# Kernel optimization log

Hardware: AMD Instinct MI355X
Metric: run time of the kernel (lower is better)

The kernel has to match this reference:

```python
import jax, jax.numpy as jnp
import numpy as np

BATCH = 8
IN_FEATURES = 4096
OUT_FEATURES = 16384


def setup_inputs() -> dict:
    key = jax.random.key(0)
    k1, k2, k3 = jax.random.split(key, 3)
    # activations, fp16 (w4a16 path)
    x = jax.random.normal(k1, (BATCH, IN_FEATURES), dtype=jnp.float16)
    # packed int4 weights: each element holds two signed 4-bit values
    # (low nibble = even column 2k, high nibble = odd column 2k+1)
    weight = jax.random.randint(k2, (OUT_FEATURES, IN_FEATURES // 2), 0, 256, dtype=jnp.int32)
    # per-output-channel symmetric scales (small positive values)
    weight_scales = (jax.random.uniform(k3, (OUT_FEATURES,), dtype=jnp.float16) * jnp.float16(0.01)
                     + jnp.float16(0.001))
    return {"x": x, "weight": weight, "weight_scales": weight_scales}


def _dequant_i4(weight, scales):
    """Unpack two signed int4 per byte and apply per-row scales.
    weight: [out, in//2] int32 (byte values 0..255); scales: [out] fp16.
    Returns [out, in] in scales.dtype.
    """
    low = weight & 0xF
    high = (weight >> 4) & 0xF
    # sign-extend 4-bit two's complement (the torch module stores signed int4;
    # mask 0x88 XOR in the kernel is the equivalent sign-bit flip)
    low = jnp.where(low >= 8, low - 16, low)
    high = jnp.where(high >= 8, high - 16, high)
    w = jnp.stack([low, high], axis=-1).reshape(weight.shape[0], -1)  # [out, in]
    return w.astype(scales.dtype) * scales[:, None]


def reference(x, weight, weight_scales):
    W = _dequant_i4(weight, weight_scales)           # [out, in] fp16
    return jnp.matmul(x, W.T)                         # [batch, out] fp16
```

## Files before the change

### kernel.cpp

```cpp
#include <hip/hip_runtime.h>
#include <stdint.h>

#define BATCH 8
#define K_DIM 4096
#define N_DIM 16384
#define KH (K_DIM / 2)
#define NPAIR (K_DIM / 2)
#define BLOCK 512
#define ROWS_PER_WAVE 4
#define ROWS_PER_BLOCK 32
#define ITERS (KH / 4 / 64)

typedef _Float16 h2 __attribute__((ext_vector_type(2)));
typedef int i4 __attribute__((ext_vector_type(4)));

__device__ __forceinline__ h2 as_h2(uint32_t u) { return __builtin_bit_cast(h2, u); }

__device__ __forceinline__ float fdot2f(h2 a, h2 b, float c) {
    return __builtin_amdgcn_fdot2(a, b, c, false);
}

__global__ __launch_bounds__(BLOCK, 4)
void w4a16_gemv(const float* __restrict__ x,
                const int*   __restrict__ w,
                const float* __restrict__ scales,
                float*       __restrict__ out)
{
    __shared__ uint4 xchunks[2 * NPAIR];
    const int tid = threadIdx.x;
    const int wave = tid >> 6;
    const int lane = tid & 63;
    const int row0 = blockIdx.x * ROWS_PER_BLOCK + wave * ROWS_PER_WAVE;

    const i4* __restrict__ wv0 = (const i4*)(w + (size_t)(row0 + 0) * KH);
    const i4* __restrict__ wv1 = (const i4*)(w + (size_t)(row0 + 1) * KH);
    const i4* __restrict__ wv2 = (const i4*)(w + (size_t)(row0 + 2) * KH);
    const i4* __restrict__ wv3 = (const i4*)(w + (size_t)(row0 + 3) * KH);

    int qwA[4][4], qwB[4][4];

    auto loadset = [&](int (&qw)[4][4], int t) {
        const int u = (t << 6) + lane;
        const i4 a = __builtin_nontemporal_load(wv0 + u);
        const i4 b = __builtin_nontemporal_load(wv1 + u);
        const i4 c = __builtin_nontemporal_load(wv2 + u);
        const i4 d = __builtin_nontemporal_load(wv3 + u);
        qw[0][0] = a[0]; qw[0][1] = a[1]; qw[0][2] = a[2]; qw[0][3] = a[3];
        qw[1][0] = b[0]; qw[1][1] = b[1]; qw[1][2] = b[2]; qw[1][3] = b[3];
        qw[2][0] = c[0]; qw[2][1] = c[1]; qw[2][2] = c[2]; qw[2][3] = c[3];
        qw[3][0] = d[0]; qw[3][1] = d[1]; qw[3][2] = d[2]; qw[3][3] = d[3];
    };

    loadset(qwA, 0);
    loadset(qwB, 1);

    #pragma unroll
    for (int it = 0; it < NPAIR / 2 / BLOCK; ++it) {
        const int q = it * BLOCK + tid;
        uint32_t pk0[BATCH], pk1[BATCH];
        #pragma unroll
        for (int b = 0; b < BATCH; ++b) {
            const float4 v = *reinterpret_cast<const float4*>(x + (size_t)b * K_DIM + 4 * q);
            pk0[b] = __builtin_bit_cast(uint32_t, __builtin_amdgcn_cvt_pkrtz(v.x, v.y));
            pk1[b] = __builtin_bit_cast(uint32_t, __builtin_amdgcn_cvt_pkrtz(v.z, v.w));
        }
        const int c0 = 4 * q;
        const int s = (q >> 1) & 7;
        xchunks[(c0 + 0) ^ s] = make_uint4(pk0[0], pk0[1], pk0[2], pk0[3]);
        xchunks[(c0 + 1) ^ s] = make_uint4(pk0[4], pk0[5], pk0[6], pk0[7]);
        xchunks[(c0 + 2) ^ s] = make_uint4(pk1[0], pk1[1], pk1[2], pk1[3]);
        xchunks[(c0 + 3) ^ s] = make_uint4(pk1[4], pk1[5], pk1[6], pk1[7]);
    }
    __syncthreads();

    float acc[ROWS_PER_WAVE][BATCH];
    #pragma unroll
    for (int j = 0; j < ROWS_PER_WAVE; ++j)
        #pragma unroll
        for (int b = 0; b < BATCH; ++b) acc[j][b] = 0.0f;

    const h2 neg1032 = as_h2(0xE408E408u);

    auto compute = [&](int (&qw)[4][4], int t) {
        const int u = (t << 6) + lane;
        const int cbase = u << 3;
        const int xork = u & 7;
        #pragma unroll
        for (int m = 0; m < 4; ++m) {
            const uint4 xa = xchunks[cbase + ((2 * m)     ^ xork)];
            const uint4 xb = xchunks[cbase + ((2 * m + 1) ^ xork)];
            #pragma unroll
            for (int j = 0; j < ROWS_PER_WAVE; ++j) {
                const uint32_t bv = (uint32_t)qw[j][m];
                const uint32_t tt = (bv & 0xFu) | ((bv << 12) & 0x000F0000u);
                const h2 w2 = as_h2(tt ^ 0x64086408u) + neg1032;
                acc[j][0] = fdot2f(w2, as_h2(xa.x), acc[j][0]);
                acc[j][1] = fdot2f(w2, as_h2(xa.y), acc[j][1]);
                acc[j][2] = fdot2f(w2, as_h2(xa.z), acc[j][2]);
                acc[j][3] = fdot2f(w2, as_h2(xa.w), acc[j][3]);
                acc[j][4] = fdot2f(w2, as_h2(xb.x), acc[j][4]);
                acc[j][5] = fdot2f(w2, as_h2(xb.y), acc[j][5]);
                acc[j][6] = fdot2f(w2, as_h2(xb.z), acc[j][6]);
                acc[j][7] = fdot2f(w2, as_h2(xb.w), acc[j][7]);
            }
        }
    };

    #pragma unroll 1
    for (int t = 0; t < ITERS - 2; t += 2) {
        compute(qwA, t);
        loadset(qwA, t + 2);
        compute(qwB, t + 1);
        loadset(qwB, t + 3);
    }
    compute(qwA, ITERS - 2);
    compute(qwB, ITERS - 1);

    float vals[32];
    #pragma unroll
    for (int j = 0; j < ROWS_PER_WAVE; ++j)
        #pragma unroll
        for (int b = 0; b < BATCH; ++b) vals[j * 8 + b] = acc[j][b];

    #pragma unroll
    for (int k = 0; k < 5; ++k) {
        const int sel = (lane >> k) & 1;
        const int n = 32 >> k;
        #pragma unroll
        for (int i = 0; i < n / 2; ++i) {
            const float a = vals[2 * i];
            const float c = vals[2 * i + 1];
            const float mine  = sel ? c : a;
            const float other = sel ? a : c;
            vals[i] = mine + __shfl_xor(other, 1 << k, 64);
        }
    }
    const float total = vals[0] + __shfl_xor(vals[0], 32, 64);

    if (lane < 32) {
        const int r = row0 + (lane >> 3);
        out[(size_t)(lane & 7) * N_DIM + r] = total * scales[r];
    }
}

extern "C" void kernel_launch(void* const* d_in, const int* in_sizes, int n_in,
                              void* d_out, int out_size, void* d_ws, size_t ws_size,
                              hipStream_t stream) {
    const float* x      = (const float*)d_in[0];
    const int*   w      = (const int*)d_in[1];
    const float* scales = (const float*)d_in[2];
    float*       out    = (float*)d_out;

    dim3 grid(N_DIM / ROWS_PER_BLOCK);
    dim3 block(BLOCK);
    hipLaunchKernelGGL(w4a16_gemv, grid, block, 0, stream, x, w, scales, out);
}
```

Baseline: 197.2 us.

## Split K across two blocks with fewer rows per wave and add reduce kernel

Each row's K dimension is now split between two blocks, and each wave handles 2 rows instead of 4. This gives four times as many blocks and higher occupancy (launch bounds raised to 8). Partial sums go to a workspace buffer, and a second kernel adds the two halves and applies the per-row scales. The trade-off is an extra launch, extra global traffic for the partials, and the x staging and conversion now being repeated in twice as many blocks.

```diff
diff --git a/kernel.cpp b/kernel.cpp
--- a/kernel.cpp
+++ b/kernel.cpp
@@ -5,11 +5,12 @@
 #define K_DIM 4096
 #define N_DIM 16384
 #define KH (K_DIM / 2)
-#define NPAIR (K_DIM / 2)
+#define KHH (KH / 2)
+#define NPAIRH (K_DIM / 4)
 #define BLOCK 512
-#define ROWS_PER_WAVE 4
-#define ROWS_PER_BLOCK 32
-#define ITERS (KH / 4 / 64)
+#define ROWS_PER_WAVE 2
+#define ROWS_PER_BLOCK 16
+#define ITERS (KHH / 4 / 64)
 
 typedef _Float16 h2 __attribute__((ext_vector_type(2)));
 typedef int i4 __attribute__((ext_vector_type(4)));
@@ -20,47 +21,41 @@
     return __builtin_amdgcn_fdot2(a, b, c, false);
 }
 
-__global__ __launch_bounds__(BLOCK, 4)
-void w4a16_gemv(const float* __restrict__ x,
-                const int*   __restrict__ w,
-                const float* __restrict__ scales,
-                float*       __restrict__ out)
+__global__ __launch_bounds__(BLOCK, 8)
+void w4a16_gemv_split(const float* __restrict__ x,
+                      const int*   __restrict__ w,
+                      float*       __restrict__ partial)
 {
-    __shared__ uint4 xchunks[2 * NPAIR];
-    const int tid = threadIdx.x;
+    __shared__ uint4 xchunks[2 * NPAIRH];
+    const int tid  = threadIdx.x;
     const int wave = tid >> 6;
     const int lane = tid & 63;
-    const int row0 = blockIdx.x * ROWS_PER_BLOCK + wave * ROWS_PER_WAVE;
+    const int z    = blockIdx.x;
+    const int half = z & 1;
+    const int row0 = (z >> 1) * ROWS_PER_BLOCK + wave * ROWS_PER_WAVE;
 
-    const i4* __restrict__ wv0 = (const i4*)(w + (size_t)(row0 + 0) * KH);
-    const i4* __restrict__ wv1 = (const i4*)(w + (size_t)(row0 + 1) * KH);
-    const i4* __restrict__ wv2 = (const i4*)(w + (size_t)(row0 + 2) * KH);
-    const i4* __restrict__ wv3 = (const i4*)(w + (size_t)(row0 + 3) * KH);
+    const i4* __restrict__ wv0 = (const i4*)(w + (size_t)(row0 + 0) * KH + half * KHH);
+    const i4* __restrict__ wv1 = (const i4*)(w + (size_t)(row0 + 1) * KH + half * KHH);
 
-    int qwA[4][4], qwB[4][4];
-
-    auto loadset = [&](int (&qw)[4][4], int t) {
+    int qwc[2][4], qwn[2][4];
+    auto loadset = [&](int (&qw)[2][4], int t) {
         const int u = (t << 6) + lane;
         const i4 a = __builtin_nontemporal_load(wv0 + u);
         const i4 b = __builtin_nontemporal_load(wv1 + u);
-        const i4 c = __builtin_nontemporal_load(wv2 + u);
-        const i4 d = __builtin_nontemporal_load(wv3 + u);
         qw[0][0] = a[0]; qw[0][1] = a[1]; qw[0][2] = a[2]; qw[0][3] = a[3];
         qw[1][0] = b[0]; qw[1][1] = b[1]; qw[1][2] = b[2]; qw[1][3] = b[3];
-        qw[2][0] = c[0]; qw[2][1] = c[1]; qw[2][2] = c[2]; qw[2][3] = c[3];
-        qw[3][0] = d[0]; qw[3][1] = d[1]; qw[3][2] = d[2]; qw[3][3] = d[3];
     };
 
-    loadset(qwA, 0);
-    loadset(qwB, 1);
+    loadset(qwc, 0);
+    loadset(qwn, 1);
 
-    #pragma unroll
-    for (int it = 0; it < NPAIR / 2 / BLOCK; ++it) {
-        const int q = it * BLOCK + tid;
+    {
+        const int q = tid;
         uint32_t pk0[BATCH], pk1[BATCH];
         #pragma unroll
         for (int b = 0; b < BATCH; ++b) {
-            const float4 v = *reinterpret_cast<const float4*>(x + (size_t)b * K_DIM + 4 * q);
+            const float4 v = *reinterpret_cast<const float4*>(
+                x + (size_t)b * K_DIM + half * (K_DIM / 2) + 4 * q);
             pk0[b] = __builtin_bit_cast(uint32_t, __builtin_amdgcn_cvt_pkrtz(v.x, v.y));
             pk1[b] = __builtin_bit_cast(uint32_t, __builtin_amdgcn_cvt_pkrtz(v.z, v.w));
         }
@@ -81,7 +76,7 @@
 
     const h2 neg1032 = as_h2(0xE408E408u);
 
-    auto compute = [&](int (&qw)[4][4], int t) {
+    auto compute = [&](int (&qw)[2][4], int t) {
         const int u = (t << 6) + lane;
         const int cbase = u << 3;
         const int xork = u & 7;
@@ -106,26 +101,23 @@
         }
     };
 
-    #pragma unroll 1
-    for (int t = 0; t < ITERS - 2; t += 2) {
-        compute(qwA, t);
-        loadset(qwA, t + 2);
-        compute(qwB, t + 1);
-        loadset(qwB, t + 3);
-    }
-    compute(qwA, ITERS - 2);
-    compute(qwB, ITERS - 1);
+    compute(qwc, 0);
+    loadset(qwc, 2);
+    compute(qwn, 1);
+    loadset(qwn, 3);
+    compute(qwc, 2);
+    compute(qwn, 3);
 
-    float vals[32];
+    float vals[16];
     #pragma unroll
     for (int j = 0; j < ROWS_PER_WAVE; ++j)
         #pragma unroll
         for (int b = 0; b < BATCH; ++b) vals[j * 8 + b] = acc[j][b];
 
     #pragma unroll
-    for (int k = 0; k < 5; ++k) {
+    for (int k = 0; k < 4; ++k) {
         const int sel = (lane >> k) & 1;
-        const int n = 32 >> k;
+        const int n = 16 >> k;
         #pragma unroll
         for (int i = 0; i < n / 2; ++i) {
             const float a = vals[2 * i];
@@ -135,12 +127,31 @@
             vals[i] = mine + __shfl_xor(other, 1 << k, 64);
         }
     }
-    const float total = vals[0] + __shfl_xor(vals[0], 32, 64);
+    const float t1 = vals[0] + __shfl_xor(vals[0], 16, 64);
+    const float total = t1 + __shfl_xor(t1, 32, 64);
 
-    if (lane < 32) {
+    if (lane < 16) {
         const int r = row0 + (lane >> 3);
-        out[(size_t)(lane & 7) * N_DIM + r] = total * scales[r];
+        partial[(size_t)((half << 3) + (lane & 7)) * N_DIM + r] = total;
     }
+}
+
+__global__ __launch_bounds__(256)
+void w4a16_reduce(const float* __restrict__ partial,
+                  const float* __restrict__ scales,
+                  float*       __restrict__ out)
+{
+    const int idx4 = (blockIdx.x * 256 + threadIdx.x) * 4;
+    const int r = idx4 & (N_DIM - 1);
+    const float4 p0 = *reinterpret_cast<const float4*>(partial + idx4);
+    const float4 p1 = *reinterpret_cast<const float4*>(partial + (size_t)BATCH * N_DIM + idx4);
+    const float4 sc = *reinterpret_cast<const float4*>(scales + r);
+    float4 o;
+    o.x = (p0.x + p1.x) * sc.x;
+    o.y = (p0.y + p1.y) * sc.y;
+    o.z = (p0.z + p1.z) * sc.z;
+    o.w = (p0.w + p1.w) * sc.w;
+    *reinterpret_cast<float4*>(out + idx4) = o;
 }
 
 extern "C" void kernel_launch(void* const* d_in, const int* in_sizes, int n_in,
@@ -150,8 +161,13 @@
     const int*   w      = (const int*)d_in[1];
     const float* scales = (const float*)d_in[2];
     float*       out    = (float*)d_out;
+    float*       part   = (float*)d_ws;
 
-    dim3 grid(N_DIM / ROWS_PER_BLOCK);
-    dim3 block(BLOCK);
-    hipLaunchKernelGGL(w4a16_gemv, grid, block, 0, stream, x, w, scales, out);
+    dim3 grid1(2 * N_DIM / ROWS_PER_BLOCK);
+    dim3 block1(BLOCK);
+    hipLaunchKernelGGL(w4a16_gemv_split, grid1, block1, 0, stream, x, w, part);
+
+    dim3 grid2(BATCH * N_DIM / 4 / 256);
+    dim3 block2(256);
+    hipLaunchKernelGGL(w4a16_reduce, grid2, block2, 0, stream, part, scales, out);
 }
```

New measurement: 193.9 us. About the same (-1.7%).

## Split K across wave pairs and halve rows per block

Applied to the files above, without the earlier changes.

Each pair of waves now shares the same four output rows, with each wave handling half of the K dimension. The partial sums are combined through shared memory after a block barrier. Rows per block drop from 32 to 16, which doubles the grid size and the number of times x is staged into LDS. The weight loads also change: they now use plain loads instead of nontemporal ones, and the double buffer becomes a single prefetch buffer. The intent is more parallelism and shorter per-wave loops, at the cost of redundant x conversion work and an extra sync.

```diff
diff --git a/kernel.cpp b/kernel.cpp
--- a/kernel.cpp
+++ b/kernel.cpp
@@ -5,11 +5,11 @@
 #define K_DIM 4096
 #define N_DIM 16384
 #define KH (K_DIM / 2)
-#define NPAIR (K_DIM / 2)
+#define KHH (KH / 2)
 #define BLOCK 512
 #define ROWS_PER_WAVE 4
-#define ROWS_PER_BLOCK 32
-#define ITERS (KH / 4 / 64)
+#define ROWS_PER_BLOCK 16
+#define ITERS (KHH / 4 / 64)
 
 typedef _Float16 h2 __attribute__((ext_vector_type(2)));
 typedef int i4 __attribute__((ext_vector_type(4)));
@@ -26,36 +26,36 @@
                 const float* __restrict__ scales,
                 float*       __restrict__ out)
 {
-    __shared__ uint4 xchunks[2 * NPAIR];
-    const int tid = threadIdx.x;
+    __shared__ uint4 xchunks[K_DIM];
+    __shared__ float sred[4][32];
+    const int tid  = threadIdx.x;
     const int wave = tid >> 6;
     const int lane = tid & 63;
-    const int row0 = blockIdx.x * ROWS_PER_BLOCK + wave * ROWS_PER_WAVE;
+    const int hh   = wave & 1;
+    const int row0 = blockIdx.x * ROWS_PER_BLOCK + (wave >> 1) * ROWS_PER_WAVE;
 
-    const i4* __restrict__ wv0 = (const i4*)(w + (size_t)(row0 + 0) * KH);
-    const i4* __restrict__ wv1 = (const i4*)(w + (size_t)(row0 + 1) * KH);
-    const i4* __restrict__ wv2 = (const i4*)(w + (size_t)(row0 + 2) * KH);
-    const i4* __restrict__ wv3 = (const i4*)(w + (size_t)(row0 + 3) * KH);
+    const i4* __restrict__ wv0 = (const i4*)(w + (size_t)(row0 + 0) * KH + hh * KHH);
+    const i4* __restrict__ wv1 = (const i4*)(w + (size_t)(row0 + 1) * KH + hh * KHH);
+    const i4* __restrict__ wv2 = (const i4*)(w + (size_t)(row0 + 2) * KH + hh * KHH);
+    const i4* __restrict__ wv3 = (const i4*)(w + (size_t)(row0 + 3) * KH + hh * KHH);
 
-    int qwA[4][4], qwB[4][4];
-
-    auto loadset = [&](int (&qw)[4][4], int t) {
+    int qw[4][4];
+    auto loadset = [&](int (&q)[4][4], int t) {
         const int u = (t << 6) + lane;
-        const i4 a = __builtin_nontemporal_load(wv0 + u);
-        const i4 b = __builtin_nontemporal_load(wv1 + u);
-        const i4 c = __builtin_nontemporal_load(wv2 + u);
-        const i4 d = __builtin_nontemporal_load(wv3 + u);
-        qw[0][0] = a[0]; qw[0][1] = a[1]; qw[0][2] = a[2]; qw[0][3] = a[3];
-        qw[1][0] = b[0]; qw[1][1] = b[1]; qw[1][2] = b[2]; qw[1][3] = b[3];
-        qw[2][0] = c[0]; qw[2][1] = c[1]; qw[2][2] = c[2]; qw[2][3] = c[3];
-        qw[3][0] = d[0]; qw[3][1] = d[1]; qw[3][2] = d[2]; qw[3][3] = d[3];
+        const i4 a = wv0[u];
+        const i4 b = wv1[u];
+        const i4 c = wv2[u];
+        const i4 d = wv3[u];
+        q[0][0] = a[0]; q[0][1] = a[1]; q[0][2] = a[2]; q[0][3] = a[3];
+        q[1][0] = b[0]; q[1][1] = b[1]; q[1][2] = b[2]; q[1][3] = b[3];
+        q[2][0] = c[0]; q[2][1] = c[1]; q[2][2] = c[2]; q[2][3] = c[3];
+        q[3][0] = d[0]; q[3][1] = d[1]; q[3][2] = d[2]; q[3][3] = d[3];
     };
 
-    loadset(qwA, 0);
-    loadset(qwB, 1);
+    loadset(qw, 0);
 
     #pragma unroll
-    for (int it = 0; it < NPAIR / 2 / BLOCK; ++it) {
+    for (int it = 0; it < K_DIM / 4 / BLOCK; ++it) {
         const int q = it * BLOCK + tid;
         uint32_t pk0[BATCH], pk1[BATCH];
         #pragma unroll
@@ -81,9 +81,10 @@
 
     const h2 neg1032 = as_h2(0xE408E408u);
 
-    auto compute = [&](int (&qw)[4][4], int t) {
+    const int coff = hh << 11;
+    auto compute = [&](int (&q)[4][4], int t) {
         const int u = (t << 6) + lane;
-        const int cbase = u << 3;
+        const int cbase = coff + (u << 3);
         const int xork = u & 7;
         #pragma unroll
         for (int m = 0; m < 4; ++m) {
@@ -91,7 +92,7 @@
             const uint4 xb = xchunks[cbase + ((2 * m + 1) ^ xork)];
             #pragma unroll
             for (int j = 0; j < ROWS_PER_WAVE; ++j) {
-                const uint32_t bv = (uint32_t)qw[j][m];
+                const uint32_t bv = (uint32_t)q[j][m];
                 const uint32_t tt = (bv & 0xFu) | ((bv << 12) & 0x000F0000u);
                 const h2 w2 = as_h2(tt ^ 0x64086408u) + neg1032;
                 acc[j][0] = fdot2f(w2, as_h2(xa.x), acc[j][0]);
@@ -107,14 +108,16 @@
     };
 
     #pragma unroll 1
-    for (int t = 0; t < ITERS - 2; t += 2) {
-        compute(qwA, t);
-        loadset(qwA, t + 2);
-        compute(qwB, t + 1);
-        loadset(qwB, t + 3);
+    for (int t = 0; t < ITERS - 1; ++t) {
+        int nq[4][4];
+        loadset(nq, t + 1);
+        compute(qw, t);
+        #pragma unroll
+        for (int j = 0; j < 4; ++j)
+            #pragma unroll
+            for (int m = 0; m < 4; ++m) qw[j][m] = nq[j][m];
     }
-    compute(qwA, ITERS - 2);
-    compute(qwB, ITERS - 1);
+    compute(qw, ITERS - 1);
 
     float vals[32];
     #pragma unroll
@@ -137,9 +140,12 @@
     }
     const float total = vals[0] + __shfl_xor(vals[0], 32, 64);
 
-    if (lane < 32) {
+    if (hh && lane < 32) sred[wave >> 1][lane] = total;
+    __syncthreads();
+    if (!hh && lane < 32) {
+        const float s2 = total + sred[wave >> 1][lane];
         const int r = row0 + (lane >> 3);
-        out[(size_t)(lane & 7) * N_DIM + r] = total * scales[r];
+        out[(size_t)(lane & 7) * N_DIM + r] = s2 * scales[r];
     }
 }
 
```

Result: no change. 197.5 us (+0.1%).
